# Kernel tuning notes

Measured on AMD Instinct MI355X. Metric: run time of the kernel, lower is better.

## Reference

```python
import jax, jax.numpy as jnp
import numpy as np

DIM = 4096
N_HEADS = 32
N_KV_HEADS = 8
HEAD_DIM = DIM // N_HEADS  # 128
B, S = 1, 2048
ROPE_THETA = 10000.0


def setup_inputs() -> dict:
    key = jax.random.key(0)
    kx, kq, kk, kv, ko = jax.random.split(key, 5)
    x = jax.random.normal(kx, (B, S, DIM), dtype=jnp.float32)
    # torch Linear weights are [out_features, in_features]
    wq = jax.random.normal(kq, (N_HEADS * HEAD_DIM, DIM), dtype=jnp.float32) * 0.02
    wk = jax.random.normal(kk, (N_KV_HEADS * HEAD_DIM, DIM), dtype=jnp.float32) * 0.02
    wv = jax.random.normal(kv, (N_KV_HEADS * HEAD_DIM, DIM), dtype=jnp.float32) * 0.02
    wo = jax.random.normal(ko, (DIM, N_HEADS * HEAD_DIM), dtype=jnp.float32) * 0.02
    # RoPE table [S, HEAD_DIM, 2]; frequencies repeated twice to match the
    # even/odd interleaved rotate_half convention of apply_rope.
    pos = jnp.arange(S, dtype=jnp.float32)
    inv_freq = 1.0 / (ROPE_THETA ** (jnp.arange(0, HEAD_DIM, 2, dtype=jnp.float32) / HEAD_DIM))
    ang = pos[:, None] * inv_freq[None, :]          # [S, HEAD_DIM/2]
    ang = jnp.repeat(ang, 2, axis=-1)               # [S, HEAD_DIM]
    rope_freqs = jnp.stack([jnp.cos(ang), jnp.sin(ang)], axis=-1)  # [S, HEAD_DIM, 2]
    return {"x": x, "wq": wq, "wk": wk, "wv": wv, "wo": wo,
            "rope_freqs": rope_freqs, "start_pos": 0}


def _rotate_half(t):
    # interleaved: (x0,x1,x2,x3,...) -> (-x1,x0,-x3,x2,...)
    t1 = t[..., ::2]
    t2 = t[..., 1::2]
    return jnp.stack((-t2, t1), axis=-1).reshape(t.shape)


def reference(x, wq, wk, wv, wo, rope_freqs, start_pos):
    b, s, _ = x.shape
    rep = N_HEADS // N_KV_HEADS
    scale = 1.0 / np.sqrt(HEAD_DIM)

    q = (x @ wq.T).reshape(b, s, N_HEADS, HEAD_DIM)
    k = (x @ wk.T).reshape(b, s, N_KV_HEADS, HEAD_DIM)
    v = (x @ wv.T).reshape(b, s, N_KV_HEADS, HEAD_DIM)

    cos = rope_freqs[..., 0][None, :, None, :]  # [1,S,1,HEAD_DIM]
    sin = rope_freqs[..., 1][None, :, None, :]
    q = q * cos + _rotate_half(q) * sin
    k = k * cos + _rotate_half(k) * sin

    # GQA without materializing repeated K/V: group query heads by kv head.
    qg = q.reshape(b, s, N_KV_HEADS, rep, HEAD_DIM)
    scores = jnp.einsum("bsgrd,btgd->bgrst", qg, k) * scale  # [B,KV,rep,S,S]
    causal = jnp.tril(jnp.ones((s, s), dtype=bool))
    scores = jnp.where(causal, scores, jnp.finfo(scores.dtype).min)
    attn = jax.nn.softmax(scores, axis=-1)
    out = jnp.einsum("bgrst,btgd->bsgrd", attn, v)           # [B,S,KV,rep,HEAD_DIM]
    out = out.reshape(b, s, N_HEADS * HEAD_DIM)
    return out @ wo.T
```

## Files before the change

kernel.cpp:

```cpp
#include <hip/hip_runtime.h>
#include <stdint.h>

#define DIM 4096
#define NH 32
#define NKV 8
#define HD 128
#define SEQ 2048
#define KVD 1024

typedef unsigned short u16;
typedef __attribute__((ext_vector_type(8))) short bf16x8;
typedef __attribute__((ext_vector_type(4))) float f32x4;

__device__ __forceinline__ float bf2f(u16 v){
  union { unsigned u; float f; } c; c.u = ((unsigned)v) << 16; return c.f;
}
__device__ __forceinline__ u16 f2bf(float f){
  union { float f; unsigned u; } c; c.f = f;
  unsigned u = c.u;
  u += 0x7FFF + ((u >> 16) & 1);
  return (u16)(u >> 16);
}
__device__ __forceinline__ unsigned pack2bf(float a, float b){
  return (unsigned)f2bf(a) | ((unsigned)f2bf(b) << 16);
}

__device__ __forceinline__ void gl_lds16(const void* g, void* l){
  __builtin_amdgcn_global_load_lds((const __attribute__((address_space(1))) void*)g,
                                   (__attribute__((address_space(3))) void*)l, 16, 0, 0);
}

#define VM4 asm volatile("s_waitcnt vmcnt(4)" ::: "memory")
#define VM2 asm volatile("s_waitcnt vmcnt(2)" ::: "memory")
#define VM0 asm volatile("s_waitcnt vmcnt(0)" ::: "memory")
#define LGKM0 asm volatile("s_waitcnt lgkmcnt(0)" ::: "memory")
#define SB0 __builtin_amdgcn_sched_barrier(0)
#define BAR __builtin_amdgcn_s_barrier()

__global__ void cvt_all(const float* __restrict__ x,  const float* __restrict__ wq,
                        const float* __restrict__ wk, const float* __restrict__ wv,
                        const float* __restrict__ wo,
                        u16* __restrict__ xb,  u16* __restrict__ wqb,
                        u16* __restrict__ wkb, u16* __restrict__ wvb,
                        u16* __restrict__ wob){
  const int b = blockIdx.x;
  const float* in; u16* out; int base;
  if      (b <  8192){ in = x;  out = xb;  base = b; }
  else if (b < 24576){ in = wq; out = wqb; base = b - 8192; }
  else if (b < 28672){ in = wk; out = wkb; base = b - 24576; }
  else if (b < 32768){ in = wv; out = wvb; base = b - 28672; }
  else               { in = wo; out = wob; base = b - 32768; }
  const int i = (base*256 + threadIdx.x)*4;
  float4 v = *(const float4*)(in + i);
  ushort4 o;
  o.x = f2bf(v.x); o.y = f2bf(v.y); o.z = f2bf(v.z); o.w = f2bf(v.w);
  *(ushort4*)(out + i) = o;
}

__global__ void add_f32(float* __restrict__ out, const float* __restrict__ p){
  const int i = blockIdx.x*256 + threadIdx.x;
  float4 a = ((const float4*)out)[i];
  const float4 b = ((const float4*)p)[i];
  a.x += b.x; a.y += b.y; a.z += b.z; a.w += b.w;
  ((float4*)out)[i] = a;
}

template<int BUNITS, int EPI>
__global__ __launch_bounds__(512, 2) void gemmP(const u16* __restrict__ A,
    const u16* __restrict__ B, void* __restrict__ C0, void* __restrict__ C1,
    void* __restrict__ C2, const float* __restrict__ rf, float* __restrict__ Cp){
  constexpr int BN = BUNITS*64;
  __shared__ __align__(16) char lds[65536 + BUNITS*16384];
  const int t = threadIdx.x, w = t >> 6, l = t & 63;
  const int lg = l >> 4, li = l & 15;
  const int wr = w >> 2, wc = w & 3;
  const int idx = ((int)blockIdx.x & 7)*32 + ((int)blockIdx.x >> 3);

  int bm, bn, kbase, nt, ks = 0;
  if (EPI == 0){ bm = idx & 7; bn = idx >> 3; kbase = 0; nt = 64; }
  else         { bm = idx & 7; ks = (idx >> 3) & 1; bn = idx >> 4; kbase = ks*2048; nt = 32; }
  const u16* Ab = A + (size_t)bm*256*DIM;
  const u16* Bb = B + (size_t)bn*BN*DIM;

  auto stA = [&](int k0, int abase, int u){
    const int r = u*64 + (t >> 3);
    gl_lds16(Ab + (size_t)r*DIM + k0 + (((t & 7) ^ (r & 7)) << 3),
             lds + abase + u*8192 + (t >> 3)*128 + (t & 7)*16);
  };
  auto stB = [&](int k0, int bbase, int u){
    const int r = u*64 + (t >> 3);
    gl_lds16(Bb + (size_t)r*DIM + k0 + (((t & 7) ^ (r & 7)) << 3),
             lds + bbase + u*8192 + (t >> 3)*128 + (t & 7)*16);
  };

  f32x4 acc[8][BUNITS] = {};
  bf16x8 bfr[BUNITS][2];

#define PH(p, ...) { \
    bf16x8 af[2][2]; \
    _Pragma("unroll") \
    for (int q = 0; q < 2; ++q){ \
      const int R = wr*128 + (2*(p)+q)*16 + li; \
      af[q][0] = *(const bf16x8*)(ldsA + R*128 + (( lg    ^ (R & 7)) << 4)); \
      af[q][1] = *(const bf16x8*)(ldsA + R*128 + (((lg+4) ^ (R & 7)) << 4)); \
    } \
    if ((p) == 0){ \
      _Pragma("unroll") \
      for (int j = 0; j < BUNITS; ++j){ \
        const int R = wc*(BUNITS*16) + j*16 + li; \
        bfr[j][0] = *(const bf16x8*)(ldsB + R*128 + (( lg    ^ (R & 7)) << 4)); \
        bfr[j][1] = *(const bf16x8*)(ldsB + R*128 + (((lg+4) ^ (R & 7)) << 4)); \
      } \
    } \
    __VA_ARGS__; \
    BAR; LGKM0; SB0; \
    __builtin_amdgcn_s_setprio(1); \
    _Pragma("unroll") \
    for (int q = 0; q < 2; ++q) \
      _Pragma("unroll") \
      for (int j = 0; j < BUNITS; ++j){ \
        acc[2*(p)+q][j] = __builtin_amdgcn_mfma_f32_16x16x32_bf16(af[q][0], bfr[j][0], acc[2*(p)+q][j], 0, 0, 0); \
        acc[2*(p)+q][j] = __builtin_amdgcn_mfma_f32_16x16x32_bf16(af[q][1], bfr[j][1], acc[2*(p)+q][j], 0, 0, 0); \
      } \
    __builtin_amdgcn_s_setprio(0); \
    BAR; }

  stA(kbase, 0, 0); stA(kbase, 0, 2);
  #pragma unroll
  for (int u = 0; u < BUNITS; ++u) stB(kbase, 65536, u);
  stA(kbase, 0, 1); stA(kbase, 0, 3);
  VM2; BAR;

  for (int tt = 0; tt < nt; ++tt){
    const int buf = tt & 1, b2 = buf ^ 1;
    const int k1 = kbase + (tt+1)*64;
    const bool pf = (tt + 1 < nt);
    const char* ldsA = lds + buf*32768;
    const char* ldsB = lds + 65536 + buf*BUNITS*8192;
    const int a2 = b2*32768, b2o = 65536 + b2*BUNITS*8192;

    PH(0, if (pf){ stA(k1, a2, 0); stA(k1, a2, 2); })
    PH(1, if (pf){ stB(k1, b2o, 0); stB(k1, b2o, 1); VM4; } else { VM0; })
    PH(2, if (pf){ if constexpr (BUNITS == 4){ stB(k1, b2o, 2); stB(k1, b2o, 3); }
                   else                      { stB(k1, b2o, 2); stA(k1, a2, 1); } })
    PH(3, if (pf){ if constexpr (BUNITS == 4){ stA(k1, a2, 1); stA(k1, a2, 3); }
                   else                      { stA(k1, a2, 3); }
                   VM2; })
  }
#undef PH

  if (EPI == 1){
    float* C = (float*)(ks ? Cp : C0);
    #pragma unroll
    for (int i = 0; i < 8; ++i){
      const int srow = bm*256 + wr*128 + i*16 + lg*4;
      #pragma unroll
      for (int j = 0; j < BUNITS; ++j){
        const int col = bn*BN + wc*(BUNITS*16) + j*16 + li;
        #pragma unroll
        for (int r = 0; r < 4; ++r)
          C[(size_t)(srow + r)*DIM + col] = acc[i][j][r];
      }
    }
  } else {
    #pragma unroll
    for (int i = 0; i < 8; ++i){
      const int srow0 = bm*256 + wr*128 + i*16 + lg*4;
      #pragma unroll
      for (int j = 0; j < BUNITS; ++j){
        const int fc0 = bn*BN + wc*(BUNITS*16) + j*16;
        const int col = fc0 + li;
        if (fc0 < 5120){
          u16* C  = (fc0 < 4096) ? (u16*)C0 : (u16*)C1;
          const int ldc  = (fc0 < 4096) ? DIM : KVD;
          const int ccol = (fc0 < 4096) ? col : col - 4096;
          const int i4 = ((col & 127) >> 1) << 2;
          #pragma unroll
          for (int r = 0; r < 4; ++r){
            const float v = acc[i][j][r];
            const float p = __shfl_xor(v, 1);
            const int srow = srow0 + r;
            const float cs = rf[(size_t)srow*256 + i4];
            const float sn = rf[(size_t)srow*256 + i4 + 1];
            const float o = (col & 1) ? (v*cs + p*sn) : (v*cs - p*sn);
            C[(size_t)srow*ldc + ccol] = f2bf(o);
          }
        } else {
          u16* C = (u16*)C2;
          ushort4 o;
          o.x = f2bf(acc[i][j][0]); o.y = f2bf(acc[i][j][1]);
          o.z = f2bf(acc[i][j][2]); o.w = f2bf(acc[i][j][3]);
          *(ushort4*)&C[(size_t)(col - 5120)*SEQ + srow0] = o;
        }
      }
    }
  }
}

__global__ __launch_bounds__(256) void flash_attn(const u16* __restrict__ Q,
                                                  const u16* __restrict__ Kg,
                                                  const u16* __restrict__ Vt,
                                                  u16* __restrict__ O){
  __shared__ bf16x8 smK[2][64*16];
  __shared__ bf16x8 smV[2][128*8];
  __shared__ __align__(16) u16 smP[4][16*64];
  const int bid = blockIdx.x;
  const int h  = bid & 31;
  const int qt = 31 - (bid >> 5);
  const int g  = h >> 2;
  const int t = threadIdx.x, w = t >> 6, l = t & 63;
  const int lg = l >> 4, li = l & 15;

  bf16x8 qf[4];
  {
    const u16* qrow = Q + (size_t)(qt*64 + w*16 + li)*DIM + h*HD;
    #pragma unroll
    for (int kc = 0; kc < 4; ++kc)
      qf[kc] = *(const bf16x8*)(qrow + kc*32 + lg*8);
  }
  f32x4 accO[8] = {};
  float mrun = -1e30f, lsum = 0.f;
  const float SC = 0.08838834764831845f * 1.4426950408889634f;

  const int ksrow = t >> 4, ksslot = t & 15;
  const int vsrow = t >> 3, vsslot = t & 7;

  auto stage = [&](int kt, int b){
    #pragma unroll
    for (int j = 0; j < 4; ++j){
      const int krow = j*16 + ksrow;
      const int ksl = (ksslot & 8) | ((ksslot ^ (krow & 7)) & 7);
      gl_lds16(Kg + (size_t)(kt*64 + krow)*KVD + g*HD + ksl*8, (char*)&smK[b][0] + j*4096 + w*1024);
      const int vrow = j*32 + vsrow;
      const int vsl = (vsslot ^ (vrow & 7)) & 7;
      gl_lds16(Vt + (size_t)(g*HD + vrow)*SEQ + kt*64 + vsl*8, (char*)&smV[b][0] + j*4096 + w*1024);
    }
  };

  stage(0, 0);
  int buf = 0;
  u16* pw = &smP[w][0];

  for (int kt = 0; kt <= qt; ++kt){
    __syncthreads();
    if (kt < qt) stage(kt + 1, buf ^ 1);

    f32x4 sacc[4] = {};
    #pragma unroll
    for (int kc = 0; kc < 4; ++kc){
      #pragma unroll
      for (int nj = 0; nj < 4; ++nj){
        const int R = nj*16 + li;
        int sl = lg + 4*kc;
        sl = (sl & 8) | ((sl ^ (R & 7)) & 7);
        sacc[nj] = __builtin_amdgcn_mfma_f32_16x16x32_bf16(smK[buf][R*16 + sl], qf[kc], sacc[nj], 0, 0, 0);
      }
    }
    float p[4][4];
    #pragma unroll
    for (int nj = 0; nj < 4; ++nj)
      #pragma unroll
      for (int r = 0; r < 4; ++r)
        p[nj][r] = sacc[nj][r] * SC;
    if (kt == qt){
      const int qloc = w*16 + li;
      #pragma unroll
      for (int nj = 0; nj < 4; ++nj)
        #pragma unroll
        for (int r = 0; r < 4; ++r)
          if (nj*16 + lg*4 + r > qloc) p[nj][r] = -1e30f;
    }
    float mx = p[0][0];
    #pragma unroll
    for (int nj = 0; nj < 4; ++nj)
      #pragma unroll
      for (int r = 0; r < 4; ++r) mx = fmaxf(mx, p[nj][r]);
    mx = fmaxf(mx, __shfl_xor(mx, 16));
    mx = fmaxf(mx, __shfl_xor(mx, 32));
    const float mnew = fmaxf(mrun, mx);
    const float alpha = exp2f(mrun - mnew);
    float s = 0.f;
    #pragma unroll
    for (int nj = 0; nj < 4; ++nj)
      #pragma unroll
      for (int r = 0; r < 4; ++r){ p[nj][r] = exp2f(p[nj][r] - mnew); s += p[nj][r]; }
    s += __shfl_xor(s, 16);
    s += __shfl_xor(s, 32);
    lsum = lsum * alpha + s;
    mrun = mnew;
    float al[4];
    #pragma unroll
    for (int r = 0; r < 4; ++r) al[r] = __shfl(alpha, (l & 48) | (lg*4 + r));
    #pragma unroll
    for (int dj = 0; dj < 8; ++dj)
      #pragma unroll
      for (int r = 0; r < 4; ++r) accO[dj][r] *= al[r];
    #pragma unroll
    for (int nj = 0; nj < 4; ++nj){
      const int c = nj*2 + (lg >> 1);
      uint2 v; v.x = pack2bf(p[nj][0], p[nj][1]); v.y = pack2bf(p[nj][2], p[nj][3]);
      *(uint2*)((char*)pw + li*128 + ((c ^ (li & 7)) << 4) + ((lg & 1) << 3)) = v;
    }
    #pragma unroll
    for (int kc2 = 0; kc2 < 2; ++kc2){
      const bf16x8 pf = *(const bf16x8*)((char*)pw + li*128 + (((kc2*4 + lg) ^ (li & 7)) << 4));
      #pragma unroll
      for (int dj = 0; dj < 8; ++dj){
        const int R = dj*16 + li;
        const bf16x8 vf = smV[buf][R*8 + ((lg + 4*kc2) ^ (R & 7))];
        accO[dj] = __builtin_amdgcn_mfma_f32_16x16x32_bf16(pf, vf, accO[dj], 0, 0, 0);
      }
    }
    buf ^= 1;
  }
  float linv[4];
  #pragma unroll
  for (int r = 0; r < 4; ++r) linv[r] = 1.f / __shfl(lsum, (l & 48) | (lg*4 + r));
  #pragma unroll
  for (int dj = 0; dj < 8; ++dj)
    #pragma unroll
    for (int r = 0; r < 4; ++r)
      O[(size_t)(qt*64 + w*16 + lg*4 + r)*DIM + h*HD + dj*16 + li] = f2bf(accO[dj][r] * linv[r]);
}

extern "C" void kernel_launch(void* const* d_in, const int* in_sizes, int n_in,
                              void* d_out, int out_size, void* d_ws, size_t ws_size,
                              hipStream_t stream){
  const float* x  = (const float*)d_in[0];
  const float* wq = (const float*)d_in[1];
  const float* wk = (const float*)d_in[2];
  const float* wv = (const float*)d_in[3];
  const float* wo = (const float*)d_in[4];
  const float* rf = (const float*)d_in[5];
  float* out = (float*)d_out;

  char* ws = (char*)d_ws;
  size_t off = 0;
  auto alloc = [&](size_t nbytes){ void* p = ws + off; off += (nbytes + 255) & ~(size_t)255; return p; };
  u16* xb  = (u16*)alloc((size_t)SEQ*DIM*2);
  u16* wqb = (u16*)alloc((size_t)DIM*DIM*2);
  u16* wkb = (u16*)alloc((size_t)KVD*DIM*2);
  u16* wvb = (u16*)alloc((size_t)KVD*DIM*2);
  u16* wob = (u16*)alloc((size_t)DIM*DIM*2);
  u16* Qb  = (u16*)alloc((size_t)SEQ*DIM*2);
  u16* K8  = (u16*)alloc((size_t)SEQ*KVD*2);
  u16* Vtr = (u16*)alloc((size_t)KVD*SEQ*2);
  u16* AO  = (u16*)alloc((size_t)SEQ*DIM*2);
  float* P1 = (float*)wqb;

  cvt_all<<<49152, 256, 0, stream>>>(x, wq, wk, wv, wo, xb, wqb, wkb, wvb, wob);

  gemmP<3, 0><<<256, 512, 0, stream>>>(xb, wqb, Qb, K8, Vtr, rf, nullptr);

  flash_attn<<<SEQ/64 * NH, 256, 0, stream>>>(Qb, K8, Vtr, AO);

  gemmP<4, 1><<<256, 512, 0, stream>>>(AO, wob, out, nullptr, nullptr, nullptr, P1);
  add_f32<<<8192, 256, 0, stream>>>(out, P1);
}
```

Before: 314.5 us.

## Switch GEMMs to 256x256 tiles with quadrant-ordered MFMA phases

Replaces the parameterized GEMM with a single 256x256 tile kernel. Each iteration runs four MFMA quadrant phases, ordered so A and B fragments are reused across adjacent phases while the next K-slice is prefetched into the other LDS buffer. The QKV projection now launches 192 blocks instead of 256, a tile mapping that aims for higher arithmetic intensity per block at the cost of fewer blocks than CUs. The output projection keeps its split-K layout but uses a new block index mapping.

Result: slower. 332.6 us (+5.8%).

```diff
diff --git a/kernel.cpp b/kernel.cpp
--- a/kernel.cpp
+++ b/kernel.cpp
@@ -30,7 +30,6 @@
                                    (__attribute__((address_space(3))) void*)l, 16, 0, 0);
 }
 
-#define VM4 asm volatile("s_waitcnt vmcnt(4)" ::: "memory")
 #define VM2 asm volatile("s_waitcnt vmcnt(2)" ::: "memory")
 #define VM0 asm volatile("s_waitcnt vmcnt(0)" ::: "memory")
 #define LGKM0 asm volatile("s_waitcnt lgkmcnt(0)" ::: "memory")
@@ -65,98 +64,113 @@
   ((float4*)out)[i] = a;
 }
 
-template<int BUNITS, int EPI>
-__global__ __launch_bounds__(512, 2) void gemmP(const u16* __restrict__ A,
+template<int EPI>
+__global__ __launch_bounds__(512, 2) void gemmQ(const u16* __restrict__ A,
     const u16* __restrict__ B, void* __restrict__ C0, void* __restrict__ C1,
     void* __restrict__ C2, const float* __restrict__ rf, float* __restrict__ Cp){
-  constexpr int BN = BUNITS*64;
-  __shared__ __align__(16) char lds[65536 + BUNITS*16384];
+  __shared__ __align__(16) char lds[131072];
   const int t = threadIdx.x, w = t >> 6, l = t & 63;
   const int lg = l >> 4, li = l & 15;
   const int wr = w >> 2, wc = w & 3;
-  const int idx = ((int)blockIdx.x & 7)*32 + ((int)blockIdx.x >> 3);
-
   int bm, bn, kbase, nt, ks = 0;
-  if (EPI == 0){ bm = idx & 7; bn = idx >> 3; kbase = 0; nt = 64; }
-  else         { bm = idx & 7; ks = (idx >> 3) & 1; bn = idx >> 4; kbase = ks*2048; nt = 32; }
+  if (EPI == 0){
+    const int idx = ((int)blockIdx.x & 7)*24 + ((int)blockIdx.x >> 3);
+    bm = idx / 24; bn = idx % 24; kbase = 0; nt = 64;
+  } else {
+    const int idx = ((int)blockIdx.x & 7)*32 + ((int)blockIdx.x >> 3);
+    bm = idx >> 5; ks = (idx >> 4) & 1; bn = idx & 15; kbase = ks*2048; nt = 32;
+  }
   const u16* Ab = A + (size_t)bm*256*DIM;
-  const u16* Bb = B + (size_t)bn*BN*DIM;
-
-  auto stA = [&](int k0, int abase, int u){
-    const int r = u*64 + (t >> 3);
-    gl_lds16(Ab + (size_t)r*DIM + k0 + (((t & 7) ^ (r & 7)) << 3),
-             lds + abase + u*8192 + (t >> 3)*128 + (t & 7)*16);
+  const u16* Bb = B + (size_t)bn*256*DIM;
+
+  auto stA = [&](int rowbase, int kabs, char* dstbuf){
+    #pragma unroll
+    for (int j = 0; j < 2; ++j){
+      const int rl = rowbase + j*64 + (t >> 3);
+      gl_lds16(Ab + (size_t)rl*DIM + kabs + (((t & 7) ^ (rl & 7)) << 3),
+               dstbuf + rl*128 + (t & 7)*16);
+    }
   };
-  auto stB = [&](int k0, int bbase, int u){
-    const int r = u*64 + (t >> 3);
-    gl_lds16(Bb + (size_t)r*DIM + k0 + (((t & 7) ^ (r & 7)) << 3),
-             lds + bbase + u*8192 + (t >> 3)*128 + (t & 7)*16);
+  auto stB = [&](int u, int kabs, char* dstbuf){
+    #pragma unroll
+    for (int j = 0; j < 2; ++j){
+      const int m = j*64 + (t >> 3);
+      const int row = ((m >> 5) << 6) + u*32 + (m & 31);
+      gl_lds16(Bb + (size_t)row*DIM + kabs + (((t & 7) ^ (row & 7)) << 3),
+               dstbuf + row*128 + (t & 7)*16);
+    }
   };
 
-  f32x4 acc[8][BUNITS] = {};
-  bf16x8 bfr[BUNITS][2];
-
-#define PH(p, ...) { \
-    bf16x8 af[2][2]; \
-    _Pragma("unroll") \
-    for (int q = 0; q < 2; ++q){ \
-      const int R = wr*128 + (2*(p)+q)*16 + li; \
-      af[q][0] = *(const bf16x8*)(ldsA + R*128 + (( lg    ^ (R & 7)) << 4)); \
-      af[q][1] = *(const bf16x8*)(ldsA + R*128 + (((lg+4) ^ (R & 7)) << 4)); \
-    } \
-    if ((p) == 0){ \
-      _Pragma("unroll") \
-      for (int j = 0; j < BUNITS; ++j){ \
-        const int R = wc*(BUNITS*16) + j*16 + li; \
-        bfr[j][0] = *(const bf16x8*)(ldsB + R*128 + (( lg    ^ (R & 7)) << 4)); \
-        bfr[j][1] = *(const bf16x8*)(ldsB + R*128 + (((lg+4) ^ (R & 7)) << 4)); \
-      } \
-    } \
-    __VA_ARGS__; \
-    BAR; LGKM0; SB0; \
+  f32x4 acc[8][4] = {};
+
+#define RDA(ms) { _Pragma("unroll") \
+    for (int i2 = 0; i2 < 4; ++i2){ \
+      const int R = wr*128 + (ms)*64 + i2*16 + li; \
+      a_[i2][0] = *(const bf16x8*)(ldsA + R*128 + (( lg    ^ (R & 7)) << 4)); \
+      a_[i2][1] = *(const bf16x8*)(ldsA + R*128 + (((lg+4) ^ (R & 7)) << 4)); } }
+#define RDB(ns, bv) { _Pragma("unroll") \
+    for (int j2 = 0; j2 < 2; ++j2){ \
+      const int R = wc*64 + (ns)*32 + j2*16 + li; \
+      bv[j2][0] = *(const bf16x8*)(ldsB + R*128 + (( lg    ^ (R & 7)) << 4)); \
+      bv[j2][1] = *(const bf16x8*)(ldsB + R*128 + (((lg+4) ^ (R & 7)) << 4)); } }
+#define MM16(ms, ns, bv) { \
     __builtin_amdgcn_s_setprio(1); \
     _Pragma("unroll") \
-    for (int q = 0; q < 2; ++q) \
+    for (int i2 = 0; i2 < 4; ++i2) \
       _Pragma("unroll") \
-      for (int j = 0; j < BUNITS; ++j){ \
-        acc[2*(p)+q][j] = __builtin_amdgcn_mfma_f32_16x16x32_bf16(af[q][0], bfr[j][0], acc[2*(p)+q][j], 0, 0, 0); \
-        acc[2*(p)+q][j] = __builtin_amdgcn_mfma_f32_16x16x32_bf16(af[q][1], bfr[j][1], acc[2*(p)+q][j], 0, 0, 0); \
-      } \
-    __builtin_amdgcn_s_setprio(0); \
-    BAR; }
-
-  stA(kbase, 0, 0); stA(kbase, 0, 2);
-  #pragma unroll
-  for (int u = 0; u < BUNITS; ++u) stB(kbase, 65536, u);
-  stA(kbase, 0, 1); stA(kbase, 0, 3);
+      for (int j2 = 0; j2 < 2; ++j2){ \
+        acc[(ms)*4+i2][(ns)*2+j2] = __builtin_amdgcn_mfma_f32_16x16x32_bf16(a_[i2][0], bv[j2][0], acc[(ms)*4+i2][(ns)*2+j2], 0, 0, 0); \
+        acc[(ms)*4+i2][(ns)*2+j2] = __builtin_amdgcn_mfma_f32_16x16x32_bf16(a_[i2][1], bv[j2][1], acc[(ms)*4+i2][(ns)*2+j2], 0, 0, 0); } \
+    __builtin_amdgcn_s_setprio(0); }
+
+  stA(  0, kbase, lds);
+  stA(128, kbase, lds);
+  stB(0, kbase, lds + 65536);
+  stB(1, kbase, lds + 65536);
   VM2; BAR;
 
   for (int tt = 0; tt < nt; ++tt){
     const int buf = tt & 1, b2 = buf ^ 1;
+    const char* ldsA = lds + buf*32768;
+    const char* ldsB = lds + 65536 + buf*32768;
+    char* ldsA2 = lds + b2*32768;
+    char* ldsB2 = lds + 65536 + b2*32768;
     const int k1 = kbase + (tt+1)*64;
     const bool pf = (tt + 1 < nt);
-    const char* ldsA = lds + buf*32768;
-    const char* ldsB = lds + 65536 + buf*BUNITS*8192;
-    const int a2 = b2*32768, b2o = 65536 + b2*BUNITS*8192;
-
-    PH(0, if (pf){ stA(k1, a2, 0); stA(k1, a2, 2); })
-    PH(1, if (pf){ stB(k1, b2o, 0); stB(k1, b2o, 1); VM4; } else { VM0; })
-    PH(2, if (pf){ if constexpr (BUNITS == 4){ stB(k1, b2o, 2); stB(k1, b2o, 3); }
-                   else                      { stB(k1, b2o, 2); stA(k1, a2, 1); } })
-    PH(3, if (pf){ if constexpr (BUNITS == 4){ stA(k1, a2, 1); stA(k1, a2, 3); }
-                   else                      { stA(k1, a2, 3); }
-                   VM2; })
-  }
-#undef PH
+    bf16x8 a_[4][2], bN0[2][2], bN1[2][2];
+
+    RDA(0); RDB(0, bN0);
+    if (pf){ stA(0, k1, ldsA2); VM2; } else { VM0; }
+    BAR; LGKM0; SB0;
+    MM16(0, 0, bN0);
+    BAR;
+    RDB(1, bN1);
+    if (pf) stA(128, k1, ldsA2);
+    BAR; LGKM0; SB0;
+    MM16(0, 1, bN1);
+    BAR;
+    RDA(1);
+    if (pf) stB(0, k1, ldsB2);
+    BAR; LGKM0; SB0;
+    MM16(1, 1, bN1);
+    BAR;
+    if (pf){ stB(1, k1, ldsB2); VM2; }
+    BAR; SB0;
+    MM16(1, 0, bN0);
+    BAR;
+  }
+#undef RDA
+#undef RDB
+#undef MM16
 
   if (EPI == 1){
     float* C = (float*)(ks ? Cp : C0);
     #pragma unroll
     for (int i = 0; i < 8; ++i){
-      const int srow = bm*256 + wr*128 + i*16 + lg*4;
-      #pragma unroll
-      for (int j = 0; j < BUNITS; ++j){
-        const int col = bn*BN + wc*(BUNITS*16) + j*16 + li;
+      const int srow = bm*256 + wr*128 + (i >> 2)*64 + (i & 3)*16 + lg*4;
+      #pragma unroll
+      for (int j = 0; j < 4; ++j){
+        const int col = bn*256 + wc*64 + (j >> 1)*32 + (j & 1)*16 + li;
         #pragma unroll
         for (int r = 0; r < 4; ++r)
           C[(size_t)(srow + r)*DIM + col] = acc[i][j][r];
@@ -165,11 +179,11 @@
   } else {
     #pragma unroll
     for (int i = 0; i < 8; ++i){
-      const int srow0 = bm*256 + wr*128 + i*16 + lg*4;
-      #pragma unroll
-      for (int j = 0; j < BUNITS; ++j){
-        const int fc0 = bn*BN + wc*(BUNITS*16) + j*16;
-        const int col = fc0 + li;
+      const int srow0 = bm*256 + wr*128 + (i >> 2)*64 + (i & 3)*16 + lg*4;
+      #pragma unroll
+      for (int j = 0; j < 4; ++j){
+        const int col = bn*256 + wc*64 + (j >> 1)*32 + (j & 1)*16 + li;
+        const int fc0 = col - li;
         if (fc0 < 5120){
           u16* C  = (fc0 < 4096) ? (u16*)C0 : (u16*)C1;
           const int ldc  = (fc0 < 4096) ? DIM : KVD;
@@ -350,10 +364,10 @@
 
   cvt_all<<<49152, 256, 0, stream>>>(x, wq, wk, wv, wo, xb, wqb, wkb, wvb, wob);
 
-  gemmP<3, 0><<<256, 512, 0, stream>>>(xb, wqb, Qb, K8, Vtr, rf, nullptr);
+  gemmQ<0><<<192, 512, 0, stream>>>(xb, wqb, Qb, K8, Vtr, rf, nullptr);
 
   flash_attn<<<SEQ/64 * NH, 256, 0, stream>>>(Qb, K8, Vtr, AO);
 
-  gemmP<4, 1><<<256, 512, 0, stream>>>(AO, wob, out, nullptr, nullptr, nullptr, P1);
+  gemmQ<1><<<256, 512, 0, stream>>>(AO, wob, out, nullptr, nullptr, nullptr, P1);
   add_f32<<<8192, 256, 0, stream>>>(out, P1);
 }
```
